# Performance work log

Hardware: AMD Instinct MI355X
Metric: run time of the kernel (lower is better)

Reference implementation:

```python
import math
import jax, jax.numpy as jnp
import numpy as np

B, S, HID = 1, 2048, 4096
NH, NKV, HD = 32, 8, 128          # query heads, kv heads, head dim (HID // NH)
G, R = NKV, NH // NKV             # kv groups, query heads per kv group
Q_SIZE, KV_SIZE = NH * HD, NKV * HD


def _get_alibi_slopes(n_heads):
    n = 2 ** math.floor(math.log2(n_heads))
    m0 = 2.0 ** (-8.0 / n)
    slopes = np.power(m0, np.arange(1, n + 1))
    if n < n_heads:
        m1 = 2.0 ** (-4.0 / n)
        mm = np.power(m1, np.arange(1, 1 + 2 * (n_heads - n), 2))
        slopes = np.concatenate([slopes, mm])
    return slopes  # NTK ratio 1.0 -> identity


def setup_inputs() -> dict:
    key = jax.random.key(0)
    k1, k2, k3 = jax.random.split(key, 3)
    positions = jnp.broadcast_to(jnp.arange(S, dtype=jnp.int32), (B, S))
    hidden_states = jax.random.normal(k1, (B, S, HID), dtype=jnp.float32)
    wqkv = jax.random.normal(k2, (Q_SIZE + 2 * KV_SIZE, HID), dtype=jnp.float32) * 0.02
    wo = jax.random.normal(k3, (HID, Q_SIZE), dtype=jnp.float32) * 0.02
    return {"positions": positions, "hidden_states": hidden_states,
            "wqkv": wqkv, "wo": wo}


def reference(positions, hidden_states, wqkv, wo):
    scale = HD ** -0.5
    slopes = jnp.asarray(_get_alibi_slopes(NH), dtype=hidden_states.dtype).reshape(G, R)

    # fused QKV projection (no bias)
    qkv = jnp.einsum('bsh,oh->bso', hidden_states, wqkv)
    q = qkv[..., :Q_SIZE].reshape(B, S, G, R, HD)
    k = qkv[..., Q_SIZE:Q_SIZE + KV_SIZE].reshape(B, S, G, HD)
    v = qkv[..., Q_SIZE + KV_SIZE:].reshape(B, S, G, HD)

    # GQA attention scores: [B, G, R, Sq, Sk]
    scores = jnp.einsum('bqgrd,bkgd->bgrqk', q, k) * scale

    # sqrt-ALiBi bias: -slope * sqrt(q_pos - k_pos), causal mask where k_pos > q_pos
    dist = positions[:, :, None] - positions[:, None, :]            # [B, Sq, Sk]
    bias = -slopes[None, :, :, None, None] * jnp.sqrt(
        jnp.maximum(dist, 0).astype(scores.dtype))[:, None, None]
    neg_inf = jnp.asarray(jnp.finfo(scores.dtype).min, scores.dtype)
    scores = jnp.where(dist[:, None, None] < 0, neg_inf, scores + bias)

    attn = jax.nn.softmax(scores, axis=-1)
    out = jnp.einsum('bgrqk,bkgd->bqgrd', attn, v).reshape(B, S, Q_SIZE)
    return jnp.einsum('bso,ho->bsh', out, wo)
```

## Files before the change

### kernel.cpp

```cpp
#include <hip/hip_runtime.h>
#include <stdint.h>

typedef __attribute__((ext_vector_type(8))) short short8;
typedef __attribute__((ext_vector_type(4))) float floatx4;

#define S_LEN 2048
#define OTOT  6144
#define KOFF  4096
#define VOFF  5120

__device__ __forceinline__ unsigned short f2bf(float f) {
  unsigned int u = __float_as_uint(f);
  u += 0x7FFFu + ((u >> 16) & 1u);
  return (unsigned short)(u >> 16);
}

__device__ __forceinline__ unsigned int pack2bf(float lo, float hi) {
  unsigned int r;
  asm("v_cvt_pk_bf16_f32 %0, %1, %2" : "=v"(r) : "v"(lo), "v"(hi));
  return r;
}

__device__ __forceinline__ void gload_lds16(const void* g, void* l) {
  __builtin_amdgcn_global_load_lds(
      (const __attribute__((address_space(1))) void*)g,
      (__attribute__((address_space(3))) void*)l, 16, 0, 0);
}

__global__ void cast_bf16_kernel(const float* __restrict__ in,
                                 unsigned short* __restrict__ out, int n4) {
  int i = blockIdx.x * blockDim.x + threadIdx.x;
  int stride = gridDim.x * blockDim.x;
  for (; i < n4; i += stride) {
    float4 v = ((const float4*)in)[i];
    ushort4 o;
    o.x = f2bf(v.x); o.y = f2bf(v.y); o.z = f2bf(v.z); o.w = f2bf(v.w);
    ((ushort4*)out)[i] = o;
  }
}

__global__ __launch_bounds__(256) void transpose_v_kernel(
    const unsigned short* __restrict__ qkv, unsigned short* __restrict__ vt) {
  __shared__ unsigned short T[128 * 74];
  int s0 = (blockIdx.x & 31) * 64;
  int g = blockIdx.x >> 5;
  int tid = threadIdx.x;
#pragma unroll
  for (int it = 0; it < 16; ++it) {
    int idx = it * 256 + tid;
    int srow = idx >> 6;
    int dc = idx & 63;
    unsigned int v = *(const unsigned int*)&qkv[(size_t)(s0 + srow) * OTOT + VOFF + g * 128 + dc * 2];
    T[(2 * dc) * 74 + srow] = (unsigned short)(v & 0xFFFF);
    T[(2 * dc + 1) * 74 + srow] = (unsigned short)(v >> 16);
  }
  __syncthreads();
#pragma unroll
  for (int it = 0; it < 16; ++it) {
    int odx = it * 256 + tid;
    int d = odx >> 5;
    int sc2 = odx & 31;
    unsigned int w = *(const unsigned int*)&T[d * 74 + 2 * sc2];
    *(unsigned int*)&vt[(size_t)(g * 128 + d) * S_LEN + s0 + 2 * sc2] = w;
  }
}

template <typename CT>
__global__ __launch_bounds__(256, 2) void gemm_bt_kernel(
    const unsigned short* __restrict__ A, const unsigned short* __restrict__ B,
    CT* __restrict__ C, int M, int N, int K) {
  __shared__ unsigned short As[128 * 64];
  __shared__ unsigned short Bs[128 * 64];

  int nbn = N >> 7;
  int nwg = gridDim.x;
  int bid = blockIdx.x;
  if ((nwg & 7) == 0) bid = (bid & 7) * (nwg >> 3) + (bid >> 3);
  int bm = bid / nbn, bn = bid % nbn;

  int tid = threadIdx.x;
  int lane = tid & 63, wave = tid >> 6;
  int lr = lane & 15, lh = lane >> 4;
  int wm = (wave >> 1) << 6, wn = (wave & 1) << 6;

  floatx4 acc[4][4];
#pragma unroll
  for (int i = 0; i < 4; ++i)
#pragma unroll
    for (int j = 0; j < 4; ++j) acc[i][j] = (floatx4){0.f, 0.f, 0.f, 0.f};

  const size_t arow = (size_t)bm * 128;
  const size_t brow = (size_t)bn * 128;
  int nk = K >> 6;
  for (int kt = 0; kt < nk; ++kt) {
#pragma unroll
    for (int i = 0; i < 4; ++i) {
      int lin = i * 4096 + tid * 16;
      int row = lin >> 7;
      int colb = (lin & 127) ^ ((row & 7) << 4);
      gload_lds16(&A[(arow + row) * K + kt * 64 + (colb >> 1)],
                  &As[(i * 4096 + wave * 1024) >> 1]);
    }
#pragma unroll
    for (int i = 0; i < 4; ++i) {
      int lin = i * 4096 + tid * 16;
      int row = lin >> 7;
      int colb = (lin & 127) ^ ((row & 7) << 4);
      gload_lds16(&B[(brow + row) * K + kt * 64 + (colb >> 1)],
                  &Bs[(i * 4096 + wave * 1024) >> 1]);
    }
    __syncthreads();
#pragma unroll
    for (int kk = 0; kk < 2; ++kk) {
      short8 af[4], bfr[4];
#pragma unroll
      for (int mi = 0; mi < 4; ++mi) {
        int row = wm + mi * 16 + lr;
        int off = (row << 7) | ((kk * 64 + lh * 16) ^ ((row & 7) << 4));
        af[mi] = *(const short8*)&As[off >> 1];
      }
#pragma unroll
      for (int ni = 0; ni < 4; ++ni) {
        int row = wn + ni * 16 + lr;
        int off = (row << 7) | ((kk * 64 + lh * 16) ^ ((row & 7) << 4));
        bfr[ni] = *(const short8*)&Bs[off >> 1];
      }
#pragma unroll
      for (int mi = 0; mi < 4; ++mi)
#pragma unroll
        for (int ni = 0; ni < 4; ++ni)
          acc[mi][ni] = __builtin_amdgcn_mfma_f32_16x16x32_bf16(
              af[mi], bfr[ni], acc[mi][ni], 0, 0, 0);
    }
    __syncthreads();
  }
#pragma unroll
  for (int mi = 0; mi < 4; ++mi)
#pragma unroll
    for (int ni = 0; ni < 4; ++ni)
#pragma unroll
      for (int r = 0; r < 4; ++r) {
        size_t grow = arow + wm + mi * 16 + lh * 4 + r;
        size_t gcol = brow + wn + ni * 16 + lr;
        float v = acc[mi][ni][r];
        if constexpr (sizeof(CT) == 2)
          ((unsigned short*)C)[grow * N + gcol] = f2bf(v);
        else
          C[grow * N + gcol] = v;
      }
}

__global__ __launch_bounds__(256, 4) void attn_kernel(
    const unsigned short* __restrict__ qkv, const unsigned short* __restrict__ vt,
    const int* __restrict__ pos, unsigned short* __restrict__ aout) {
  __shared__ unsigned short Klds[64 * 128];
  __shared__ unsigned short Vlds[128 * 64];

  int bid = blockIdx.x;
  int h = bid & 31;
  int qt = 31 - (bid >> 5);
  int g = h >> 2;
  const float L2E = 1.4426950408889634f;
  float slope2 = exp2f(-0.25f * (float)(h + 1)) * L2E;
  const float QS2 = 0.08838834764831845f * L2E;
  const float THR = 8.0f * L2E;

  int tid = threadIdx.x, lane = tid & 63, wave = tid >> 6;
  int lr = lane & 15, lh = lane >> 4;
  int qrow0 = qt * 64 + wave * 16;

  short8 qf[4];
#pragma unroll
  for (int kk = 0; kk < 4; ++kk)
    qf[kk] = *(const short8*)&qkv[(size_t)(qrow0 + lr) * OTOT + h * 128 + kk * 32 + lh * 8];
  int qpos = pos[qrow0 + lr];

  float m_run = -3.0e38f, l_run = 0.f;
  floatx4 acc[8];
#pragma unroll
  for (int n = 0; n < 8; ++n) acc[n] = (floatx4){0.f, 0.f, 0.f, 0.f};

  for (int jj = 0; jj <= qt; ++jj) {
    int j = qt - jj;
    int kbase = j * 64;
#pragma unroll
    for (int i = 0; i < 4; ++i) {
      int lin = i * 4096 + tid * 16;
      int row = lin >> 8;
      int colb = (lin & 255) ^ (((row >> 1) & 7) << 4);
      gload_lds16(&qkv[(size_t)(kbase + row) * OTOT + KOFF + g * 128 + (colb >> 1)],
                  &Klds[(i * 4096 + wave * 1024) >> 1]);
    }
#pragma unroll
    for (int i = 0; i < 4; ++i) {
      int lin = i * 4096 + tid * 16;
      int row = lin >> 7;
      int colb = (lin & 127) ^ ((row & 7) << 4);
      gload_lds16(&vt[(size_t)(g * 128 + row) * S_LEN + kbase + (colb >> 1)],
                  &Vlds[(i * 4096 + wave * 1024) >> 1]);
    }
    __syncthreads();

    floatx4 sc[4];
#pragma unroll
    for (int n = 0; n < 4; ++n) sc[n] = (floatx4){0.f, 0.f, 0.f, 0.f};
#pragma unroll
    for (int n = 0; n < 4; ++n) {
      int rowk = 32 * (n & 1) + 2 * lr + (n >> 1);
      int swz = ((rowk >> 1) & 7) << 4;
#pragma unroll
      for (int kk = 0; kk < 4; ++kk) {
        short8 kf = *(const short8*)&Klds[((rowk << 8) | ((kk * 64 + lh * 16) ^ swz)) >> 1];
        sc[n] = __builtin_amdgcn_mfma_f32_16x16x32_bf16(kf, qf[kk], sc[n], 0, 0, 0);
      }
    }

    int4 a0 = *(const int4*)&pos[kbase + lh * 8];
    int4 a1 = *(const int4*)&pos[kbase + lh * 8 + 4];
    int4 b0 = *(const int4*)&pos[kbase + 32 + lh * 8];
    int4 b1 = *(const int4*)&pos[kbase + 32 + lh * 8 + 4];
    int klo[8] = {a0.x, a0.y, a0.z, a0.w, a1.x, a1.y, a1.z, a1.w};
    int khi[8] = {b0.x, b0.y, b0.z, b0.w, b1.x, b1.y, b1.z, b1.w};

#pragma unroll
    for (int n = 0; n < 4; ++n)
#pragma unroll
      for (int r = 0; r < 4; ++r) {
        int jidx = 2 * r + (n >> 1);
        int kp = (n & 1) ? khi[jidx] : klo[jidx];
        int dist = qpos - kp;
        float sv = sc[n][r] * QS2 - slope2 * sqrtf((float)dist);
        sc[n][r] = (dist < 0) ? -1.0e38f : sv;
      }

    float mx = sc[0][0];
#pragma unroll
    for (int n = 0; n < 4; ++n)
#pragma unroll
      for (int r = 0; r < 4; ++r) mx = fmaxf(mx, sc[n][r]);
    mx = fmaxf(mx, __shfl_xor(mx, 16));
    mx = fmaxf(mx, __shfl_xor(mx, 32));

    if (__any(mx > m_run + THR)) {
      float mnew = fmaxf(m_run, mx);
      float al = exp2f(m_run - mnew);
      l_run *= al;
#pragma unroll
      for (int n = 0; n < 8; ++n) acc[n] *= al;
      m_run = mnew;
    }

    float rs = 0.f;
    union { unsigned int u[4]; short8 v; } pf0, pf1;
#pragma unroll
    for (int w = 0; w < 4; ++w) {
      float e0 = exp2f(sc[0][w] - m_run);
      float e2 = exp2f(sc[2][w] - m_run);
      float e1 = exp2f(sc[1][w] - m_run);
      float e3 = exp2f(sc[3][w] - m_run);
      rs += (e0 + e2) + (e1 + e3);
      pf0.u[w] = pack2bf(e0, e2);
      pf1.u[w] = pack2bf(e1, e3);
    }
    rs += __shfl_xor(rs, 16);
    rs += __shfl_xor(rs, 32);
    l_run += rs;

#pragma unroll
    for (int n = 0; n < 8; ++n) {
      int rowv = n * 16 + lr;
      int swz = (rowv & 7) << 4;
      short8 v0 = *(const short8*)&Vlds[((rowv << 7) | ((lh * 16) ^ swz)) >> 1];
      short8 v1 = *(const short8*)&Vlds[((rowv << 7) | ((64 + lh * 16) ^ swz)) >> 1];
      acc[n] = __builtin_amdgcn_mfma_f32_16x16x32_bf16(v0, pf0.v, acc[n], 0, 0, 0);
      acc[n] = __builtin_amdgcn_mfma_f32_16x16x32_bf16(v1, pf1.v, acc[n], 0, 0, 0);
    }
    __syncthreads();
  }

  float inv = 1.0f / l_run;
#pragma unroll
  for (int n = 0; n < 8; ++n) {
    ushort4 o;
    o.x = f2bf(acc[n][0] * inv);
    o.y = f2bf(acc[n][1] * inv);
    o.z = f2bf(acc[n][2] * inv);
    o.w = f2bf(acc[n][3] * inv);
    *(ushort4*)&aout[(size_t)(qrow0 + lr) * 4096 + h * 128 + n * 16 + lh * 4] = o;
  }
}

extern "C" void kernel_launch(void* const* d_in, const int* in_sizes, int n_in,
                              void* d_out, int out_size, void* d_ws, size_t ws_size,
                              hipStream_t stream) {
  (void)in_sizes; (void)n_in; (void)out_size;
  const int* positions = (const int*)d_in[0];
  const float* hidden = (const float*)d_in[1];
  const float* wqkv = (const float*)d_in[2];
  const float* wo = (const float*)d_in[3];
  float* out = (float*)d_out;

  char* w = (char*)d_ws;
  unsigned short* hbf   = (unsigned short*)(w);
  unsigned short* wqbf  = (unsigned short*)(w + 16777216);
  unsigned short* wobf  = (unsigned short*)(w + 67108864);
  unsigned short* qkv   = (unsigned short*)(w + 100663296);
  unsigned short* vtb   = (unsigned short*)(w + 125829120);
  unsigned short* attnb = (unsigned short*)(w + 130023424);
  if (ws_size < 146800640) return;

  cast_bf16_kernel<<<2048, 256, 0, stream>>>(hidden, hbf, 2048 * 4096 / 4);
  cast_bf16_kernel<<<2048, 256, 0, stream>>>(wqkv, wqbf, 6144 * 4096 / 4);
  cast_bf16_kernel<<<2048, 256, 0, stream>>>(wo, wobf, 4096 * 4096 / 4);

  gemm_bt_kernel<unsigned short><<<768, 256, 0, stream>>>(hbf, wqbf, qkv, 2048, 6144, 4096);
  transpose_v_kernel<<<256, 256, 0, stream>>>(qkv, vtb);
  attn_kernel<<<1024, 256, 0, stream>>>(qkv, vtb, positions, attnb);
  gemm_bt_kernel<float><<<512, 256, 0, stream>>>(attnb, wobf, out, 2048, 4096, 4096);
}
```

Measured before the change: 519.0 us.

## Share GQA K/V tiles across a group's four heads and fuse cast kernels

The attention kernel now maps one block to a KV group, with each of the four waves handling one query head of that group over 32 query rows. Each K/V tile loaded into LDS is therefore reused by all four heads instead of being reloaded per head, and the grid is halved. The causal tile ordering is reworked to interleave long and short query tiles, and s_setprio is raised around the MFMA sections. The three fp32-to-bf16 cast launches are merged into one kernel. In exchange, each wave holds twice the accumulator and score state and occupancy is lowered to 2 blocks per SIMD via launch bounds, which risks register pressure and less latency hiding.

```diff
diff --git a/kernel.cpp b/kernel.cpp
--- a/kernel.cpp
+++ b/kernel.cpp
@@ -27,15 +27,30 @@
       (__attribute__((address_space(3))) void*)l, 16, 0, 0);
 }
 
-__global__ void cast_bf16_kernel(const float* __restrict__ in,
-                                 unsigned short* __restrict__ out, int n4) {
-  int i = blockIdx.x * blockDim.x + threadIdx.x;
-  int stride = gridDim.x * blockDim.x;
-  for (; i < n4; i += stride) {
-    float4 v = ((const float4*)in)[i];
-    ushort4 o;
-    o.x = f2bf(v.x); o.y = f2bf(v.y); o.z = f2bf(v.z); o.w = f2bf(v.w);
-    ((ushort4*)out)[i] = o;
+__global__ void cast3_kernel(const float* __restrict__ ha, const float* __restrict__ wq,
+                             const float* __restrict__ wo_,
+                             unsigned short* __restrict__ oh,
+                             unsigned short* __restrict__ owq,
+                             unsigned short* __restrict__ owo) {
+  int i0 = blockIdx.x * 256 + threadIdx.x;
+  int stride = gridDim.x * 256;
+#pragma unroll 1
+  for (int i = i0; i < 2097152; i += stride) {
+    float4 v = ((const float4*)ha)[i];
+    ushort4 o; o.x = f2bf(v.x); o.y = f2bf(v.y); o.z = f2bf(v.z); o.w = f2bf(v.w);
+    ((ushort4*)oh)[i] = o;
+  }
+#pragma unroll 1
+  for (int i = i0; i < 6291456; i += stride) {
+    float4 v = ((const float4*)wq)[i];
+    ushort4 o; o.x = f2bf(v.x); o.y = f2bf(v.y); o.z = f2bf(v.z); o.w = f2bf(v.w);
+    ((ushort4*)owq)[i] = o;
+  }
+#pragma unroll 1
+  for (int i = i0; i < 4194304; i += stride) {
+    float4 v = ((const float4*)wo_)[i];
+    ushort4 o; o.x = f2bf(v.x); o.y = f2bf(v.y); o.z = f2bf(v.z); o.w = f2bf(v.w);
+    ((ushort4*)owo)[i] = o;
   }
 }
 
@@ -150,38 +165,47 @@
       }
 }
 
-__global__ __launch_bounds__(256, 4) void attn_kernel(
+__global__ __launch_bounds__(256, 2) void attn_kernel(
     const unsigned short* __restrict__ qkv, const unsigned short* __restrict__ vt,
     const int* __restrict__ pos, unsigned short* __restrict__ aout) {
   __shared__ unsigned short Klds[64 * 128];
   __shared__ unsigned short Vlds[128 * 64];
 
-  int bid = blockIdx.x;
-  int h = bid & 31;
-  int qt = 31 - (bid >> 5);
-  int g = h >> 2;
+  int b = blockIdx.x;
+  int g = b & 7;
+  int rr = b >> 3;
+  int qt = (rr < 32) ? (63 - rr) : (rr - 32);
+
+  int tid = threadIdx.x, lane = tid & 63, wave = tid >> 6;
+  int lr = lane & 15, lh = lane >> 4;
+  int h = g * 4 + wave;
+
   const float L2E = 1.4426950408889634f;
   float slope2 = exp2f(-0.25f * (float)(h + 1)) * L2E;
   const float QS2 = 0.08838834764831845f * L2E;
   const float THR = 8.0f * L2E;
 
-  int tid = threadIdx.x, lane = tid & 63, wave = tid >> 6;
-  int lr = lane & 15, lh = lane >> 4;
-  int qrow0 = qt * 64 + wave * 16;
-
-  short8 qf[4];
-#pragma unroll
-  for (int kk = 0; kk < 4; ++kk)
-    qf[kk] = *(const short8*)&qkv[(size_t)(qrow0 + lr) * OTOT + h * 128 + kk * 32 + lh * 8];
-  int qpos = pos[qrow0 + lr];
-
-  float m_run = -3.0e38f, l_run = 0.f;
-  floatx4 acc[8];
-#pragma unroll
-  for (int n = 0; n < 8; ++n) acc[n] = (floatx4){0.f, 0.f, 0.f, 0.f};
-
-  for (int jj = 0; jj <= qt; ++jj) {
-    int j = qt - jj;
+  int qrow0 = qt * 32;
+
+  short8 qf[2][4];
+#pragma unroll
+  for (int qc = 0; qc < 2; ++qc)
+#pragma unroll
+    for (int kk = 0; kk < 4; ++kk)
+      qf[qc][kk] = *(const short8*)&qkv[(size_t)(qrow0 + qc * 16 + lr) * OTOT +
+                                        h * 128 + kk * 32 + lh * 8];
+  int qpos[2] = {pos[qrow0 + lr], pos[qrow0 + 16 + lr]};
+
+  float m_run[2] = {-3.0e38f, -3.0e38f}, l_run[2] = {0.f, 0.f};
+  floatx4 acc[8][2];
+#pragma unroll
+  for (int n = 0; n < 8; ++n)
+#pragma unroll
+    for (int qc = 0; qc < 2; ++qc) acc[n][qc] = (floatx4){0.f, 0.f, 0.f, 0.f};
+
+  int nkt = (qt >> 1) + 1;
+  for (int jj = 0; jj < nkt; ++jj) {
+    int j = nkt - 1 - jj;
     int kbase = j * 64;
 #pragma unroll
     for (int i = 0; i < 4; ++i) {
@@ -201,9 +225,12 @@
     }
     __syncthreads();
 
-    floatx4 sc[4];
-#pragma unroll
-    for (int n = 0; n < 4; ++n) sc[n] = (floatx4){0.f, 0.f, 0.f, 0.f};
+    floatx4 sc[4][2];
+#pragma unroll
+    for (int n = 0; n < 4; ++n)
+#pragma unroll
+      for (int qc = 0; qc < 2; ++qc) sc[n][qc] = (floatx4){0.f, 0.f, 0.f, 0.f};
+    __builtin_amdgcn_s_setprio(1);
 #pragma unroll
     for (int n = 0; n < 4; ++n) {
       int rowk = 32 * (n & 1) + 2 * lr + (n >> 1);
@@ -211,9 +238,11 @@
 #pragma unroll
       for (int kk = 0; kk < 4; ++kk) {
         short8 kf = *(const short8*)&Klds[((rowk << 8) | ((kk * 64 + lh * 16) ^ swz)) >> 1];
-        sc[n] = __builtin_amdgcn_mfma_f32_16x16x32_bf16(kf, qf[kk], sc[n], 0, 0, 0);
-      }
-    }
+        sc[n][0] = __builtin_amdgcn_mfma_f32_16x16x32_bf16(kf, qf[0][kk], sc[n][0], 0, 0, 0);
+        sc[n][1] = __builtin_amdgcn_mfma_f32_16x16x32_bf16(kf, qf[1][kk], sc[n][1], 0, 0, 0);
+      }
+    }
+    __builtin_amdgcn_s_setprio(0);
 
     int4 a0 = *(const int4*)&pos[kbase + lh * 8];
     int4 a1 = *(const int4*)&pos[kbase + lh * 8 + 4];
@@ -222,71 +251,94 @@
     int klo[8] = {a0.x, a0.y, a0.z, a0.w, a1.x, a1.y, a1.z, a1.w};
     int khi[8] = {b0.x, b0.y, b0.z, b0.w, b1.x, b1.y, b1.z, b1.w};
 
+    float mx[2] = {-3.0e38f, -3.0e38f};
 #pragma unroll
     for (int n = 0; n < 4; ++n)
 #pragma unroll
-      for (int r = 0; r < 4; ++r) {
-        int jidx = 2 * r + (n >> 1);
+      for (int rj = 0; rj < 4; ++rj) {
+        int jidx = 2 * rj + (n >> 1);
         int kp = (n & 1) ? khi[jidx] : klo[jidx];
-        int dist = qpos - kp;
-        float sv = sc[n][r] * QS2 - slope2 * sqrtf((float)dist);
-        sc[n][r] = (dist < 0) ? -1.0e38f : sv;
-      }
-
-    float mx = sc[0][0];
-#pragma unroll
-    for (int n = 0; n < 4; ++n)
-#pragma unroll
-      for (int r = 0; r < 4; ++r) mx = fmaxf(mx, sc[n][r]);
-    mx = fmaxf(mx, __shfl_xor(mx, 16));
-    mx = fmaxf(mx, __shfl_xor(mx, 32));
-
-    if (__any(mx > m_run + THR)) {
-      float mnew = fmaxf(m_run, mx);
-      float al = exp2f(m_run - mnew);
-      l_run *= al;
-#pragma unroll
-      for (int n = 0; n < 8; ++n) acc[n] *= al;
-      m_run = mnew;
-    }
-
-    float rs = 0.f;
-    union { unsigned int u[4]; short8 v; } pf0, pf1;
+#pragma unroll
+        for (int qc = 0; qc < 2; ++qc) {
+          int dist = qpos[qc] - kp;
+          float sv = sc[n][qc][rj] * QS2 - slope2 * sqrtf((float)dist);
+          sv = (dist < 0) ? -1.0e38f : sv;
+          sc[n][qc][rj] = sv;
+          mx[qc] = fmaxf(mx[qc], sv);
+        }
+      }
+#pragma unroll
+    for (int qc = 0; qc < 2; ++qc) {
+      mx[qc] = fmaxf(mx[qc], __shfl_xor(mx[qc], 16));
+      mx[qc] = fmaxf(mx[qc], __shfl_xor(mx[qc], 32));
+    }
+
+    bool nd = (mx[0] > m_run[0] + THR) | (mx[1] > m_run[1] + THR);
+    if (__any(nd)) {
+#pragma unroll
+      for (int qc = 0; qc < 2; ++qc) {
+        float mnew = fmaxf(m_run[qc], mx[qc]);
+        float al = exp2f(m_run[qc] - mnew);
+        l_run[qc] *= al;
+#pragma unroll
+        for (int n = 0; n < 8; ++n) acc[n][qc] *= al;
+        m_run[qc] = mnew;
+      }
+    }
+
+    union bfp { unsigned int u[4]; short8 v; };
+    bfp pfA0, pfA1, pfB0, pfB1;
+    float rs0 = 0.f, rs1 = 0.f;
 #pragma unroll
     for (int w = 0; w < 4; ++w) {
-      float e0 = exp2f(sc[0][w] - m_run);
-      float e2 = exp2f(sc[2][w] - m_run);
-      float e1 = exp2f(sc[1][w] - m_run);
-      float e3 = exp2f(sc[3][w] - m_run);
-      rs += (e0 + e2) + (e1 + e3);
-      pf0.u[w] = pack2bf(e0, e2);
-      pf1.u[w] = pack2bf(e1, e3);
-    }
-    rs += __shfl_xor(rs, 16);
-    rs += __shfl_xor(rs, 32);
-    l_run += rs;
-
+      float e0 = exp2f(sc[0][0][w] - m_run[0]);
+      float e2 = exp2f(sc[2][0][w] - m_run[0]);
+      float e1 = exp2f(sc[1][0][w] - m_run[0]);
+      float e3 = exp2f(sc[3][0][w] - m_run[0]);
+      rs0 += (e0 + e2) + (e1 + e3);
+      pfA0.u[w] = pack2bf(e0, e2);
+      pfA1.u[w] = pack2bf(e1, e3);
+      float f0 = exp2f(sc[0][1][w] - m_run[1]);
+      float f2 = exp2f(sc[2][1][w] - m_run[1]);
+      float f1 = exp2f(sc[1][1][w] - m_run[1]);
+      float f3 = exp2f(sc[3][1][w] - m_run[1]);
+      rs1 += (f0 + f2) + (f1 + f3);
+      pfB0.u[w] = pack2bf(f0, f2);
+      pfB1.u[w] = pack2bf(f1, f3);
+    }
+    rs0 += __shfl_xor(rs0, 16); rs0 += __shfl_xor(rs0, 32);
+    rs1 += __shfl_xor(rs1, 16); rs1 += __shfl_xor(rs1, 32);
+    l_run[0] += rs0;
+    l_run[1] += rs1;
+
+    __builtin_amdgcn_s_setprio(1);
 #pragma unroll
     for (int n = 0; n < 8; ++n) {
       int rowv = n * 16 + lr;
       int swz = (rowv & 7) << 4;
       short8 v0 = *(const short8*)&Vlds[((rowv << 7) | ((lh * 16) ^ swz)) >> 1];
       short8 v1 = *(const short8*)&Vlds[((rowv << 7) | ((64 + lh * 16) ^ swz)) >> 1];
-      acc[n] = __builtin_amdgcn_mfma_f32_16x16x32_bf16(v0, pf0.v, acc[n], 0, 0, 0);
-      acc[n] = __builtin_amdgcn_mfma_f32_16x16x32_bf16(v1, pf1.v, acc[n], 0, 0, 0);
-    }
+      acc[n][0] = __builtin_amdgcn_mfma_f32_16x16x32_bf16(v0, pfA0.v, acc[n][0], 0, 0, 0);
+      acc[n][0] = __builtin_amdgcn_mfma_f32_16x16x32_bf16(v1, pfA1.v, acc[n][0], 0, 0, 0);
+      acc[n][1] = __builtin_amdgcn_mfma_f32_16x16x32_bf16(v0, pfB0.v, acc[n][1], 0, 0, 0);
+      acc[n][1] = __builtin_amdgcn_mfma_f32_16x16x32_bf16(v1, pfB1.v, acc[n][1], 0, 0, 0);
+    }
+    __builtin_amdgcn_s_setprio(0);
     __syncthreads();
   }
 
-  float inv = 1.0f / l_run;
-#pragma unroll
-  for (int n = 0; n < 8; ++n) {
-    ushort4 o;
-    o.x = f2bf(acc[n][0] * inv);
-    o.y = f2bf(acc[n][1] * inv);
-    o.z = f2bf(acc[n][2] * inv);
-    o.w = f2bf(acc[n][3] * inv);
-    *(ushort4*)&aout[(size_t)(qrow0 + lr) * 4096 + h * 128 + n * 16 + lh * 4] = o;
+#pragma unroll
+  for (int qc = 0; qc < 2; ++qc) {
+    float inv = 1.0f / l_run[qc];
+#pragma unroll
+    for (int n = 0; n < 8; ++n) {
+      ushort4 o;
+      o.x = f2bf(acc[n][qc][0] * inv);
+      o.y = f2bf(acc[n][qc][1] * inv);
+      o.z = f2bf(acc[n][qc][2] * inv);
+      o.w = f2bf(acc[n][qc][3] * inv);
+      *(ushort4*)&aout[(size_t)(qrow0 + qc * 16 + lr) * 4096 + h * 128 + n * 16 + lh * 4] = o;
+    }
   }
 }
 
@@ -309,12 +361,9 @@
   unsigned short* attnb = (unsigned short*)(w + 130023424);
   if (ws_size < 146800640) return;
 
-  cast_bf16_kernel<<<2048, 256, 0, stream>>>(hidden, hbf, 2048 * 4096 / 4);
-  cast_bf16_kernel<<<2048, 256, 0, stream>>>(wqkv, wqbf, 6144 * 4096 / 4);
-  cast_bf16_kernel<<<2048, 256, 0, stream>>>(wo, wobf, 4096 * 4096 / 4);
-
+  cast3_kernel<<<2048, 256, 0, stream>>>(hidden, wqkv, wo, hbf, wqbf, wobf);
   gemm_bt_kernel<unsigned short><<<768, 256, 0, stream>>>(hbf, wqbf, qkv, 2048, 6144, 4096);
   transpose_v_kernel<<<256, 256, 0, stream>>>(qkv, vtb);
-  attn_kernel<<<1024, 256, 0, stream>>>(qkv, vtb, positions, attnb);
+  attn_kernel<<<512, 256, 0, stream>>>(qkv, vtb, positions, attnb);
   gemm_bt_kernel<float><<<512, 256, 0, stream>>>(attnb, wobf, out, 2048, 4096, 4096);
 }
```

New measurement: 535.9 us. 3.2% more time.
